# Performance work log

Measured on AMD Instinct MI355X. Metric: run time of the kernel, lower is better.

The kernel has to match this reference:

```python
import jax, jax.numpy as jnp
import numpy as np

B, S, D = 8, 2048, 256


def setup_inputs() -> dict:
    key = jax.random.key(0)
    ks = jax.random.split(key, 8)
    nodes = jax.random.normal(ks[0], (B, S, D), dtype=jnp.float32)
    mask = jax.random.randint(ks[1], (B, S), 0, 2, dtype=jnp.int32)
    # ensure at least one unmasked position per row to avoid all--inf softmax
    mask = mask.at[:, 0].set(1)
    scale = 1.0 / np.sqrt(D)
    Wq = jax.random.normal(ks[2], (D, D), dtype=jnp.float32) * scale
    bq = jnp.zeros((D,), dtype=jnp.float32)
    Wk = jax.random.normal(ks[3], (D, D), dtype=jnp.float32) * scale
    bk = jnp.zeros((D,), dtype=jnp.float32)
    Wv = jax.random.normal(ks[4], (D, D), dtype=jnp.float32) * scale
    bv = jnp.zeros((D,), dtype=jnp.float32)
    return {"nodes": nodes, "mask": mask, "Wq": Wq, "bq": bq,
            "Wk": Wk, "bk": bk, "Wv": Wv, "bv": bv}


def reference(nodes, mask, Wq, bq, Wk, bk, Wv, bv):
    # Linear layers: x @ W.T + b (torch nn.Linear convention)
    q = jnp.einsum('bsd,ed->bse', nodes, Wq) + bq   # [B,S,D]
    k = jnp.einsum('bsd,ed->bse', nodes, Wk) + bk
    v = jnp.einsum('bsd,ed->bse', nodes, Wv) + bv
    d = k.shape[-1]
    scores = jnp.einsum('bqd,bkd->bqk', q, k) / jnp.sqrt(jnp.float32(d))  # [B,S,S]
    # mask[b, j] == 0 masks key column j for every query row
    scores = jnp.where(mask[:, None, :] != 0, scores, -jnp.inf)
    attn = jax.nn.softmax(scores, axis=-1)           # [B,S,S]
    weighted = jnp.einsum('bqk,bkd->bqd', attn, v)   # [B,S,D]
    return jnp.mean(weighted, axis=1)                # [B,D]
```

## Files before the change

kernel.cpp:

```cpp
#include <hip/hip_runtime.h>
#include <hip/hip_bf16.h>
#include <stdint.h>


typedef short short8 __attribute__((ext_vector_type(8)));
typedef float floatx4 __attribute__((ext_vector_type(4)));

#define MFMA16(a, b, c) __builtin_amdgcn_mfma_f32_16x16x32_bf16((a), (b), (c), 0, 0, 0)

#define ASYNC16(gsrc, ldst)                                                    \
    __builtin_amdgcn_global_load_lds(                                          \
        (__attribute__((address_space(1))) void*)(void*)(gsrc),                \
        (__attribute__((address_space(3))) void*)(ldst), 16, 0, 0)

static __device__ __forceinline__ unsigned short f2bf(float f) {
    union { float f; unsigned u; } v; v.f = f;
    unsigned r = v.u + 0x7fffu + ((v.u >> 16) & 1u);
    return (unsigned short)(r >> 16);
}
static __device__ __forceinline__ float bf2f(unsigned short h) {
    union { unsigned u; float f; } v; v.u = ((unsigned)h) << 16;
    return v.f;
}

__global__ __launch_bounds__(64) void k_compact(
    const int* __restrict__ mask, int* __restrict__ cidx, int* __restrict__ cnt)
{
    int b = blockIdx.x, lane = threadIdx.x;
    int base = 0;
    for (int c = 0; c < 2048; c += 64) {
        int m = mask[b * 2048 + c + lane];
        unsigned long long bal = __ballot(m != 0);
        int pre = __popcll(bal & ((1ull << lane) - 1ull));
        if (m) cidx[b * 2048 + base + pre] = c + lane;
        base += __popcll(bal);
    }
    if (lane == 0) cnt[b] = base;
    for (int i = base + lane; i < 2048; i += 64) cidx[b * 2048 + i] = 0;
}

__global__ __launch_bounds__(256) void k_convert(
    const float* __restrict__ nodes, const float* __restrict__ Wq,
    const float* __restrict__ Wk, const float* __restrict__ Wv,
    unsigned short* __restrict__ nbf, unsigned short* __restrict__ wbf)
{
    int unit = blockIdx.x * 256 + threadIdx.x;
    const float* src;
    unsigned short* dst;
    int off;
    if (unit < 524288) {
        src = nodes; dst = nbf; off = unit * 8;
    } else {
        int j = (unit - 524288) * 8;
        int m = j >> 16;
        int r = j & 65535;
        src = (m == 0) ? Wq : (m == 1 ? Wk : Wv);
        dst = wbf + m * 65536;
        off = r;
    }
    float4 a = *(const float4*)(src + off);
    float4 b = *(const float4*)(src + off + 4);
    short8 o;
    o[0] = f2bf(a.x); o[1] = f2bf(a.y); o[2] = f2bf(a.z); o[3] = f2bf(a.w);
    o[4] = f2bf(b.x); o[5] = f2bf(b.y); o[6] = f2bf(b.z); o[7] = f2bf(b.w);
    *(short8*)(dst + off) = o;
}

__global__ __launch_bounds__(256) void k_proj2(
    const unsigned short* __restrict__ nbf,
    const unsigned short* __restrict__ wbf,
    const float* __restrict__ bq, const float* __restrict__ bk,
    const float* __restrict__ bv,
    unsigned short* __restrict__ qb, unsigned short* __restrict__ kb,
    unsigned short* __restrict__ vb)
{
    __shared__ unsigned short As[128 * 64];
    __shared__ unsigned short Bs[128 * 64];
    int tid = threadIdx.x, lane = tid & 63, wave = tid >> 6;
    int wm = wave & 1, wn = wave >> 1;
    int l15 = lane & 15, quad = lane >> 4;
    int mBase = blockIdx.x * 128;
    int nBase = blockIdx.y * 128;
    int z = blockIdx.z;
    const unsigned short* W = wbf + z * 65536;

    floatx4 acc[4][4] = {};

    int srow[4], scol[4];
#pragma unroll
    for (int i = 0; i < 4; ++i) {
        int p = i * 256 + tid;
        srow[i] = p >> 3;
        scol[i] = (p & 7) ^ (srow[i] & 7);
    }

    for (int kc = 0; kc < 256; kc += 64) {
#pragma unroll
        for (int i = 0; i < 4; ++i) {
            int p = i * 256 + tid;
            *(short8*)(&As[p * 8]) =
                *(const short8*)(nbf + (mBase + srow[i]) * 256 + kc + scol[i] * 8);
            *(short8*)(&Bs[p * 8]) =
                *(const short8*)(W + (nBase + srow[i]) * 256 + kc + scol[i] * 8);
        }
        __syncthreads();
#pragma unroll
        for (int ks = 0; ks < 2; ++ks) {
            int c8 = ks * 4 + quad;
            short8 af[4], bfr[4];
#pragma unroll
            for (int i = 0; i < 4; ++i) {
                int row = wm * 64 + i * 16 + l15;
                af[i] = *(const short8*)(&As[(row * 8 + (c8 ^ (row & 7))) * 8]);
            }
#pragma unroll
            for (int i = 0; i < 4; ++i) {
                int row = wn * 64 + i * 16 + l15;
                bfr[i] = *(const short8*)(&Bs[(row * 8 + (c8 ^ (row & 7))) * 8]);
            }
#pragma unroll
            for (int mi = 0; mi < 4; ++mi)
#pragma unroll
                for (int ni = 0; ni < 4; ++ni)
                    acc[mi][ni] = MFMA16(af[mi], bfr[ni], acc[mi][ni]);
        }
        __syncthreads();
    }

    const float* bias = (z == 0) ? bq : (z == 1 ? bk : bv);
    unsigned short* out = (z == 0) ? qb : (z == 1 ? kb : vb);
    float scale = (z == 0) ? 0.0625f : 1.0f;
#pragma unroll
    for (int mi = 0; mi < 4; ++mi)
#pragma unroll
        for (int ni = 0; ni < 4; ++ni) {
            int col = nBase + wn * 64 + ni * 16 + l15;
            float bval = bias[col];
#pragma unroll
            for (int r = 0; r < 4; ++r) {
                int row = mBase + wm * 64 + mi * 16 + quad * 4 + r;
                out[row * 256 + col] = f2bf((acc[mi][ni][r] + bval) * scale);
            }
        }
}

__global__ __launch_bounds__(256) void k_repack(
    const unsigned short* __restrict__ kb, const int* __restrict__ cidx,
    const int* __restrict__ cnt_g, unsigned short* __restrict__ kbt)
{
    int c = blockIdx.x, b = blockIdx.y;
    int cnt = cnt_g[b];
    if (c * 64 >= cnt) return;
    size_t obase = ((size_t)b * 32 + c) * 16384;
#pragma unroll
    for (int i = 0; i < 8; ++i) {
        int idx = i * 256 + threadIdx.x;
        int du = idx >> 6, key = idx & 63;
        int krow = cidx[b * 2048 + c * 64 + key];
        short8 v = *(const short8*)(kb + ((size_t)b * 2048 + krow) * 256 + du * 8);
        *(short8*)(kbt + obase + (size_t)idx * 8) = v;
    }
}

__global__ __launch_bounds__(256) void k_pass1t(
    const unsigned short* __restrict__ qb, const unsigned short* __restrict__ kbt,
    const int* __restrict__ cnt_g, float* __restrict__ lsum_g,
    unsigned short* __restrict__ pbuf)
{
    __shared__ unsigned short kt[16384];
    int tid = threadIdx.x, lane = tid & 63, wave = tid >> 6;
    int l15 = lane & 15, quad = lane >> 4;
    int b = blockIdx.z;
    int cnt = cnt_g[b];
    int nchunk = (cnt + 63) >> 6;
    int qBase = blockIdx.x * 128 + wave * 32;
    int qcg = blockIdx.x * 4 + wave;

    short8 qf[2][8];
#pragma unroll
    for (int mi = 0; mi < 2; ++mi)
#pragma unroll
        for (int ks = 0; ks < 8; ++ks)
            qf[mi][ks] = *(const short8*)(qb + (b * 2048 + qBase + mi * 16 + l15) * 256 + ks * 32 + quad * 8);

    float ls[2][4] = {};
    for (int c = blockIdx.y; c < nchunk; c += 4) {
        const unsigned short* src = kbt + ((size_t)b * 32 + c) * 16384;
#pragma unroll
        for (int i = 0; i < 8; ++i) {
            int seg = wave * 8 + i;
            ASYNC16(src + seg * 512 + lane * 8, &kt[seg * 512]);
        }
        __syncthreads();
#pragma unroll
        for (int nt = 0; nt < 4; ++nt) {
            short8 kf[8];
#pragma unroll
            for (int ks = 0; ks < 8; ++ks)
                kf[ks] = *(const short8*)(&kt[((ks * 4 + quad) * 64 + nt * 16 + l15) * 8]);
            floatx4 acc[2] = {};
#pragma unroll
            for (int ks = 0; ks < 8; ++ks) {
                acc[0] = MFMA16(qf[0][ks], kf[ks], acc[0]);
                acc[1] = MFMA16(qf[1][ks], kf[ks], acc[1]);
            }
            float bias = (c * 64 + nt * 16 + l15 < cnt) ? 0.0f : -1e30f;
            short8 hh;
#pragma unroll
            for (int mi = 0; mi < 2; ++mi)
#pragma unroll
                for (int r = 0; r < 4; ++r) {
                    float e = __expf(acc[mi][r] + bias);
                    ls[mi][r] += e;
                    union { _Float16 h; short s; } u; u.h = (_Float16)e;
                    hh[mi * 4 + r] = u.s;
                }
            int ktile = c * 4 + nt;
            if (ktile < 96) {
                size_t off = ((((size_t)b * 96 + ktile) * 64 + qcg) * 64 + lane) * 8;
                *(short8*)(pbuf + off) = hh;
            }
        }
        __syncthreads();
    }
#pragma unroll
    for (int mi = 0; mi < 2; ++mi)
#pragma unroll
        for (int r = 0; r < 4; ++r) {
            float v = ls[mi][r];
            v += __shfl_xor(v, 1); v += __shfl_xor(v, 2);
            v += __shfl_xor(v, 4); v += __shfl_xor(v, 8);
            if (l15 == 0)
                atomicAdd(&lsum_g[b * 2048 + qBase + mi * 16 + quad * 4 + r], v);
        }
}

__global__ __launch_bounds__(512) void k_wred4(
    const unsigned short* __restrict__ pbuf, const float* __restrict__ lsum_g,
    const int* __restrict__ cidx, const int* __restrict__ cnt_g,
    float* __restrict__ wsum_g)
{
    __shared__ float linv_p[2048];
    int tid = threadIdx.x, lane = tid & 63, wave = tid >> 6;
    int l15 = lane & 15, quad = lane >> 4;
    int b = blockIdx.z;
    int ktile = blockIdx.y * 8 + wave;

#pragma unroll
    for (int i = 0; i < 4; ++i) {
        int idx = i * 512 + tid;
        int qcg = idx >> 5, qd = (idx >> 3) & 3, j = idx & 7;
        int q = qcg * 32 + (j >> 2) * 16 + qd * 4 + (j & 3);
        linv_p[idx] = 1.0f / lsum_g[b * 2048 + q];
    }
    __syncthreads();

    int cnt = cnt_g[b];
    if (ktile >= 96 || ktile * 16 >= cnt) return;

    int qcg0 = blockIdx.x * 32;
    float acc = 0.f;
#pragma unroll 4
    for (int qcg = qcg0; qcg < qcg0 + 32; ++qcg) {
        size_t off = ((((size_t)b * 96 + ktile) * 64 + qcg) * 64 + lane) * 8;
        short8 pv = *(const short8*)(pbuf + off);
        const float* lv = &linv_p[(qcg * 4 + quad) * 8];
        floatx4 l0 = *(const floatx4*)lv;
        floatx4 l1 = *(const floatx4*)(lv + 4);
#pragma unroll
        for (int j = 0; j < 4; ++j) {
            union { short s; _Float16 h; } u0, u1;
            u0.s = pv[j]; u1.s = pv[4 + j];
            acc += (float)u0.h * l0[j] + (float)u1.h * l1[j];
        }
    }
    acc += __shfl_xor(acc, 16);
    acc += __shfl_xor(acc, 32);
    int slot = ktile * 16 + l15;
    if (lane < 16 && slot < cnt)
        atomicAdd(&wsum_g[b * 2048 + cidx[b * 2048 + slot]], acc);
}

__global__ __launch_bounds__(256) void k_out(
    const float* __restrict__ wsum_g, const unsigned short* __restrict__ vb,
    float* __restrict__ outp)
{
    int b = blockIdx.y;
    int d = threadIdx.x;
    int k0 = blockIdx.x * 128;
    float acc = 0.f;
#pragma unroll 4
    for (int k = k0; k < k0 + 128; ++k) {
        float wv = wsum_g[b * 2048 + k];
        acc += wv * bf2f(vb[(b * 2048 + k) * 256 + d]);
    }
    atomicAdd(&outp[b * 256 + d], acc * (1.0f / 2048.0f));
}

extern "C" void kernel_launch(void* const* d_in, const int* in_sizes, int n_in,
                              void* d_out, int out_size, void* d_ws, size_t ws_size,
                              hipStream_t stream)
{
    const float* nodes = (const float*)d_in[0];
    const int*   mask  = (const int*)d_in[1];
    const float* Wq    = (const float*)d_in[2];
    const float* bq    = (const float*)d_in[3];
    const float* Wk    = (const float*)d_in[4];
    const float* bk    = (const float*)d_in[5];
    const float* Wv    = (const float*)d_in[6];
    const float* bv    = (const float*)d_in[7];
    float* out = (float*)d_out;

    unsigned short* qb  = (unsigned short*)d_ws;
    unsigned short* kb  = qb + 4194304;
    unsigned short* vb  = kb + 4194304;
    float* lsum = (float*)(vb + 4194304);
    float* wsum = lsum + 16384;
    int*   cnt  = (int*)(wsum + 16384);
    int*   cidx = cnt + 16;
    unsigned short* kbt = (unsigned short*)(cidx + 16384);
    unsigned short* X   = kbt + 4194304;
    unsigned short* nbf = X;
    unsigned short* wbf = X + 4194304;
    unsigned short* pbuf = X;

    hipMemsetAsync(lsum, 0, 32768 * sizeof(float), stream);
    hipMemsetAsync(d_out, 0, 2048 * sizeof(float), stream);

    k_compact<<<8, 64, 0, stream>>>(mask, cidx, cnt);
    k_convert<<<2144, 256, 0, stream>>>(nodes, Wq, Wk, Wv, nbf, wbf);
    k_proj2<<<dim3(128, 2, 3), 256, 0, stream>>>(nbf, wbf, bq, bk, bv, qb, kb, vb);
    k_repack<<<dim3(32, 8), 256, 0, stream>>>(kb, cidx, cnt, kbt);
    k_pass1t<<<dim3(16, 4, 8), 256, 0, stream>>>(qb, kbt, cnt, lsum, pbuf);
    k_wred4<<<dim3(2, 16, 8), 512, 0, stream>>>(pbuf, lsum, cidx, cnt, wsum);
    k_out<<<dim3(16, 8), 256, 0, stream>>>(wsum, vb, out);
}
```

Before: 151.5 us.

## Fold memsets into compact kernel and use async global-to-LDS loads in projection

Drops the two hipMemsetAsync calls and zeroes the lsum/wsum buffers and the output inside extra blocks of the mask-compaction kernel, removing separate launches. The projection GEMM now loads its tiles with global_load_lds 16-byte direct-to-LDS transfers instead of going through registers with ordinary loads and stores, keeping the XOR swizzle by remapping the global source addresses. This depends on the per-wave contiguous LDS destination layout being correct for the async instruction. The load is still followed immediately by a barrier, so there is no real overlap.

```diff
diff --git a/kernel.cpp b/kernel.cpp
--- a/kernel.cpp
+++ b/kernel.cpp
@@ -23,20 +23,36 @@
     return v.f;
 }
 
-__global__ __launch_bounds__(64) void k_compact(
-    const int* __restrict__ mask, int* __restrict__ cidx, int* __restrict__ cnt)
-{
-    int b = blockIdx.x, lane = threadIdx.x;
-    int base = 0;
-    for (int c = 0; c < 2048; c += 64) {
-        int m = mask[b * 2048 + c + lane];
-        unsigned long long bal = __ballot(m != 0);
-        int pre = __popcll(bal & ((1ull << lane) - 1ull));
-        if (m) cidx[b * 2048 + base + pre] = c + lane;
-        base += __popcll(bal);
-    }
-    if (lane == 0) cnt[b] = base;
-    for (int i = base + lane; i < 2048; i += 64) cidx[b * 2048 + i] = 0;
+__global__ __launch_bounds__(256) void k_compact2(
+    const int* __restrict__ mask, int* __restrict__ cidx, int* __restrict__ cnt,
+    float* __restrict__ zbase ,
+    float* __restrict__ outp )
+{
+    int blk = blockIdx.x;
+    if (blk < 8) {
+        if (threadIdx.x < 64) {
+            int b = blk, lane = threadIdx.x;
+            int base = 0;
+            for (int c = 0; c < 2048; c += 64) {
+                int m = mask[b * 2048 + c + lane];
+                unsigned long long bal = __ballot(m != 0);
+                int pre = __popcll(bal & ((1ull << lane) - 1ull));
+                if (m) cidx[b * 2048 + base + pre] = c + lane;
+                base += __popcll(bal);
+            }
+            if (lane == 0) cnt[b] = base;
+            for (int i = base + lane; i < 2048; i += 64) cidx[b * 2048 + i] = 0;
+        }
+        return;
+    }
+    int idx = (blk - 8) * 256 + threadIdx.x;
+    float4 z = {0.f, 0.f, 0.f, 0.f};
+#pragma unroll
+    for (int j = 0; j < 2; ++j) {
+        int p = idx + j * 4352;
+        if (p < 8192) ((float4*)zbase)[p] = z;
+        else ((float4*)outp)[p - 8192] = z;
+    }
 }
 
 __global__ __launch_bounds__(256) void k_convert(
@@ -66,7 +82,7 @@
     *(short8*)(dst + off) = o;
 }
 
-__global__ __launch_bounds__(256) void k_proj2(
+__global__ __launch_bounds__(256) void k_proj2a(
     const unsigned short* __restrict__ nbf,
     const unsigned short* __restrict__ wbf,
     const float* __restrict__ bq, const float* __restrict__ bk,
@@ -74,8 +90,8 @@
     unsigned short* __restrict__ qb, unsigned short* __restrict__ kb,
     unsigned short* __restrict__ vb)
 {
-    __shared__ unsigned short As[128 * 64];
-    __shared__ unsigned short Bs[128 * 64];
+    __shared__ __align__(16) unsigned short As[128 * 64];
+    __shared__ __align__(16) unsigned short Bs[128 * 64];
     int tid = threadIdx.x, lane = tid & 63, wave = tid >> 6;
     int wm = wave & 1, wn = wave >> 1;
     int l15 = lane & 15, quad = lane >> 4;
@@ -86,22 +102,17 @@
 
     floatx4 acc[4][4] = {};
 
-    int srow[4], scol[4];
-#pragma unroll
-    for (int i = 0; i < 4; ++i) {
-        int p = i * 256 + tid;
-        srow[i] = p >> 3;
-        scol[i] = (p & 7) ^ (srow[i] & 7);
-    }
-
     for (int kc = 0; kc < 256; kc += 64) {
 #pragma unroll
         for (int i = 0; i < 4; ++i) {
-            int p = i * 256 + tid;
-            *(short8*)(&As[p * 8]) =
-                *(const short8*)(nbf + (mBase + srow[i]) * 256 + kc + scol[i] * 8);
-            *(short8*)(&Bs[p * 8]) =
-                *(const short8*)(W + (nBase + srow[i]) * 256 + kc + scol[i] * 8);
+            int p = i * 256 + wave * 64 + lane;
+            int row = p >> 3;
+            int col8 = (p & 7) ^ (row & 7);
+            int goff = row * 256 + kc + col8 * 8;
+            unsigned short* dstA = &As[(i * 256 + wave * 64) * 8];
+            unsigned short* dstB = &Bs[(i * 256 + wave * 64) * 8];
+            ASYNC16(nbf + mBase * 256 + goff, dstA);
+            ASYNC16(W + nBase * 256 + goff, dstB);
         }
         __syncthreads();
 #pragma unroll
@@ -167,7 +178,7 @@
     const int* __restrict__ cnt_g, float* __restrict__ lsum_g,
     unsigned short* __restrict__ pbuf)
 {
-    __shared__ unsigned short kt[16384];
+    __shared__ __align__(16) unsigned short kt[16384];
     int tid = threadIdx.x, lane = tid & 63, wave = tid >> 6;
     int l15 = lane & 15, quad = lane >> 4;
     int b = blockIdx.z;
@@ -324,12 +335,9 @@
     unsigned short* wbf = X + 4194304;
     unsigned short* pbuf = X;
 
-    hipMemsetAsync(lsum, 0, 32768 * sizeof(float), stream);
-    hipMemsetAsync(d_out, 0, 2048 * sizeof(float), stream);
-
-    k_compact<<<8, 64, 0, stream>>>(mask, cidx, cnt);
+    k_compact2<<<25, 256, 0, stream>>>(mask, cidx, cnt, lsum, out);
     k_convert<<<2144, 256, 0, stream>>>(nodes, Wq, Wk, Wv, nbf, wbf);
-    k_proj2<<<dim3(128, 2, 3), 256, 0, stream>>>(nbf, wbf, bq, bk, bv, qb, kb, vb);
+    k_proj2a<<<dim3(128, 2, 3), 256, 0, stream>>>(nbf, wbf, bq, bk, bv, qb, kb, vb);
     k_repack<<<dim3(32, 8), 256, 0, stream>>>(kb, cidx, cnt, kbt);
     k_pass1t<<<dim3(16, 4, 8), 256, 0, stream>>>(qb, kbt, cnt, lsum, pbuf);
     k_wred4<<<dim3(2, 16, 8), 512, 0, stream>>>(pbuf, lsum, cidx, cnt, wsum);
```

After: 146.4 us. 1.03x faster.
